# Optimization experiments

Measured on AMD Instinct MI355X. Metric: run time of the kernel, lower is better.

The kernel has to match this reference:

```python
import jax, jax.numpy as jnp
import numpy as np


def setup_inputs() -> dict:
    key = jax.random.key(0)
    k1, k2 = jax.random.split(key)
    B, N, M, C = 4, 8192, 8192, 3
    ref = jax.random.normal(k1, (B, N, C), dtype=jnp.float32)
    query = jax.random.normal(k2, (B, M, C), dtype=jnp.float32)
    return {"ref": ref, "query": query, "k": 16}


def reference(ref, query, k):
    # ref:   [B, N, C] reference points
    # query: [B, M, C] query points
    # Squared Euclidean distances via ||q||^2 + ||r||^2 - 2 q.r  -> [B, M, N]
    q_sq = jnp.sum(query * query, axis=-1, keepdims=True)          # [B, M, 1]
    r_sq = jnp.sum(ref * ref, axis=-1)[:, None, :]                 # [B, 1, N]
    cross = jnp.einsum("bmc,bnc->bmn", query, ref)                 # [B, M, N]
    d2 = jnp.maximum(q_sq + r_sq - 2.0 * cross, 0.0)
    # k smallest distances, sorted ascending (knn_cuda convention)
    neg_topk, idx = jax.lax.top_k(-d2, k)                          # [B, M, k]
    dist = jnp.sqrt(-neg_topk)
    return dist, idx
```

## Files before the change

### kernel.cpp

```cpp
#include <hip/hip_runtime.h>


#define TPB 128
#define QPB 16
#define SPL 8
#define KK 16
#define TILE_PTS 512
#define CAP 16
#define TRIG 8

typedef unsigned long long u64k;
typedef float f32x2 __attribute__((ext_vector_type(2)));

__device__ __forceinline__ f32x2 pk_mul(f32x2 a, f32x2 b) {
  f32x2 d;
  asm("v_pk_mul_f32 %0, %1, %2" : "=v"(d) : "v"(a), "v"(b));
  return d;
}
__device__ __forceinline__ f32x2 pk_fma(f32x2 a, f32x2 b, f32x2 c) {
  f32x2 d;
  asm("v_pk_fma_f32 %0, %1, %2, %3" : "=v"(d) : "v"(a), "v"(b), "v"(c));
  return d;
}
__device__ __forceinline__ f32x2 pk_add(f32x2 a, f32x2 b) {
  f32x2 d;
  asm("v_pk_add_f32 %0, %1, %2" : "=v"(d) : "v"(a), "v"(b));
  return d;
}

#define CE(x, i, j)                                   \
  {                                                   \
    u64k ki_ = x[i], kj_ = x[j];                      \
    bool c_ = kj_ < ki_;                              \
    x[i] = c_ ? kj_ : ki_;                            \
    x[j] = c_ ? ki_ : kj_;                            \
  }

__device__ __forceinline__ void sort16(u64k x[KK]) {
  CE(x,0,1) CE(x,2,3) CE(x,4,5) CE(x,6,7) CE(x,8,9) CE(x,10,11) CE(x,12,13) CE(x,14,15)
  CE(x,0,2) CE(x,1,3) CE(x,4,6) CE(x,5,7) CE(x,8,10) CE(x,9,11) CE(x,12,14) CE(x,13,15)
  CE(x,1,2) CE(x,5,6) CE(x,9,10) CE(x,13,14)
  CE(x,0,4) CE(x,1,5) CE(x,2,6) CE(x,3,7) CE(x,8,12) CE(x,9,13) CE(x,10,14) CE(x,11,15)
  CE(x,2,4) CE(x,3,5) CE(x,10,12) CE(x,11,13)
  CE(x,1,2) CE(x,3,4) CE(x,5,6) CE(x,9,10) CE(x,11,12) CE(x,13,14)
  CE(x,0,8) CE(x,1,9) CE(x,2,10) CE(x,3,11) CE(x,4,12) CE(x,5,13) CE(x,6,14) CE(x,7,15)
  CE(x,4,8) CE(x,5,9) CE(x,6,10) CE(x,7,11)
  CE(x,2,4) CE(x,3,5) CE(x,6,8) CE(x,7,9) CE(x,10,12) CE(x,11,13)
  CE(x,1,2) CE(x,3,4) CE(x,5,6) CE(x,7,8) CE(x,9,10) CE(x,11,12) CE(x,13,14)
}

__device__ __forceinline__ void mergeTop16(u64k a[KK], u64k e[KK]) {
#pragma unroll
  for (int i = 0; i < KK; ++i) {
    u64k bv = e[KK - 1 - i];
    if (bv < a[i]) a[i] = bv;
  }
  CE(a,0,8) CE(a,1,9) CE(a,2,10) CE(a,3,11) CE(a,4,12) CE(a,5,13) CE(a,6,14) CE(a,7,15)
  CE(a,0,4) CE(a,1,5) CE(a,2,6) CE(a,3,7) CE(a,8,12) CE(a,9,13) CE(a,10,14) CE(a,11,15)
  CE(a,0,2) CE(a,1,3) CE(a,4,6) CE(a,5,7) CE(a,8,10) CE(a,9,11) CE(a,12,14) CE(a,13,15)
  CE(a,0,1) CE(a,2,3) CE(a,4,5) CE(a,6,7) CE(a,8,9) CE(a,10,11) CE(a,12,13) CE(a,14,15)
}

__global__ __launch_bounds__(TPB, 4) void knn_topk_kernel(
    const float* __restrict__ ref, const float* __restrict__ query,
    float* __restrict__ dout, float* __restrict__ iout, int N, int M) {
#pragma clang fp contract(off)
  __shared__ float tx[TILE_PTS], ty[TILE_PTS], tz[TILE_PTS], tw[TILE_PTS];
  __shared__ unsigned int sd[CAP * TPB];
  __shared__ unsigned short sg[CAP * TPB];

  float4* tx4 = (float4*)tx;
  float4* ty4 = (float4*)ty;
  float4* tz4 = (float4*)tz;
  float4* tw4 = (float4*)tw;

  const int tid = threadIdx.x;
  const int h = tid & (SPL - 1);
  const int qid = blockIdx.x * QPB + (tid >> 3);
  const int b = qid / M;

  const float* qp = query + (size_t)qid * 3;
  const float qx = qp[0], qy = qp[1], qz = qp[2];
  const float q2 = (qx * qx + qz * qz) + qy * qy;
  const f32x2 qxx = {qx, qx}, qyy = {qy, qy}, qzz = {qz, qz};
  const f32x2 q22 = {q2, q2}, n22 = {-2.0f, -2.0f};

  u64k kl[KK];
  float T;
  int cnt = 0;

  const float* refb = ref + (size_t)b * N * 3;

  auto compact = [&]() {
    u64k e[KK];
#pragma unroll
    for (int s = 0; s < KK; ++s) {
      unsigned int db = sd[s * TPB + tid];
      unsigned int gi = sg[s * TPB + tid];
      u64k key = ((u64k)db << 32) | gi;
      e[s] = (s < cnt) ? key : ~0ull;
    }
    sort16(e);
    mergeTop16(kl, e);
    cnt = 0;
    float a15 = __uint_as_float((unsigned)(kl[KK - 1] >> 32));
    float m = fminf(a15, __shfl_xor(a15, 1));
    m = fminf(m, __shfl_xor(m, 2));
    T = fminf(m, __shfl_xor(m, 4));
  };

  auto evalg = [&](int j, f32x2& d01, f32x2& d23) {
    int ridx = (h << 4) + (j ^ h);
    float4 xs = tx4[ridx];
    float4 ys = ty4[ridx];
    float4 zs = tz4[ridx];
    float4 ws = tw4[ridx];
    f32x2 x01 = {xs.x, xs.y}, x23 = {xs.z, xs.w};
    f32x2 y01 = {ys.x, ys.y}, y23 = {ys.z, ys.w};
    f32x2 z01 = {zs.x, zs.y}, z23 = {zs.z, zs.w};
    f32x2 w01 = {ws.x, ws.y}, w23 = {ws.z, ws.w};
    f32x2 cr01 = pk_mul(qxx, x01);
    cr01 = pk_fma(qyy, y01, cr01);
    cr01 = pk_fma(qzz, z01, cr01);
    f32x2 s01 = pk_add(q22, w01);
    d01 = pk_fma(n22, cr01, s01);
    f32x2 cr23 = pk_mul(qxx, x23);
    cr23 = pk_fma(qyy, y23, cr23);
    cr23 = pk_fma(qzz, z23, cr23);
    f32x2 s23 = pk_add(q22, w23);
    d23 = pk_fma(n22, cr23, s23);
  };

  auto app = [&](float d2, int gi) {
    if (d2 <= T) {
      float d2c = d2 < 0.f ? 0.f : d2;
      sd[cnt * TPB + tid] = __float_as_uint(d2c);
      sg[cnt * TPB + tid] = (unsigned short)gi;
      cnt++;
    }
  };

  const int ntiles = N / TILE_PTS;
  for (int t = 0; t < ntiles; ++t) {
    __syncthreads();
    {
      int pl = tid * 4;
      const float4* rp =
          (const float4*)(refb + (size_t)(t * TILE_PTS + pl) * 3);
      float4 f0 = rp[0], f1 = rp[1], f2 = rp[2];
      float x0 = f0.x, y0 = f0.y, z0 = f0.z;
      float x1 = f0.w, y1 = f1.x, z1 = f1.y;
      float x2 = f1.z, y2 = f1.w, z2 = f2.x;
      float x3 = f2.y, y3 = f2.z, z3 = f2.w;
      int widx = ((tid >> 4) << 4) + ((tid & 15) ^ (tid >> 4));
      tx4[widx] = make_float4(x0, x1, x2, x3);
      ty4[widx] = make_float4(y0, y1, y2, y3);
      tz4[widx] = make_float4(z0, z1, z2, z3);
      tw4[widx] = make_float4((x0 * x0 + z0 * z0) + y0 * y0,
                              (x1 * x1 + z1 * z1) + y1 * y1,
                              (x2 * x2 + z2 * z2) + y2 * y2,
                              (x3 * x3 + z3 * z3) + y3 * y3);
    }
    __syncthreads();
    const int tbase = t * TILE_PTS;
    int j0 = 0;
    if (t == 0) {
#pragma unroll
      for (int j = 0; j < 4; ++j) {
        f32x2 d01, d23;
        evalg(j, d01, d23);
        int gb = (h << 6) + (j << 2);
        float v0 = d01.x < 0.f ? 0.f : d01.x;
        float v1 = d01.y < 0.f ? 0.f : d01.y;
        float v2 = d23.x < 0.f ? 0.f : d23.x;
        float v3 = d23.y < 0.f ? 0.f : d23.y;
        kl[j * 4 + 0] = ((u64k)__float_as_uint(v0) << 32) | (unsigned)(gb + 0);
        kl[j * 4 + 1] = ((u64k)__float_as_uint(v1) << 32) | (unsigned)(gb + 1);
        kl[j * 4 + 2] = ((u64k)__float_as_uint(v2) << 32) | (unsigned)(gb + 2);
        kl[j * 4 + 3] = ((u64k)__float_as_uint(v3) << 32) | (unsigned)(gb + 3);
      }
      sort16(kl);
      float a15 = __uint_as_float((unsigned)(kl[KK - 1] >> 32));
      float m = fminf(a15, __shfl_xor(a15, 1));
      m = fminf(m, __shfl_xor(m, 2));
      T = fminf(m, __shfl_xor(m, 4));
      j0 = 4;
    }
    for (int j = j0; j < TILE_PTS / SPL / 4; j += 2) {
      {
        f32x2 d01, d23;
        evalg(j, d01, d23);
        int gb = tbase + (h << 6) + (j << 2);
        app(d01.x, gb + 0);
        app(d01.y, gb + 1);
        app(d23.x, gb + 2);
        app(d23.y, gb + 3);
      }
      {
        f32x2 d01, d23;
        evalg(j + 1, d01, d23);
        int gb = tbase + (h << 6) + ((j + 1) << 2);
        app(d01.x, gb + 0);
        app(d01.y, gb + 1);
        app(d23.x, gb + 2);
        app(d23.y, gb + 3);
      }
      if (__any(cnt >= TRIG)) compact();
    }
  }
  if (__any(cnt > 0)) compact();

#pragma unroll
  for (int d = 1; d < SPL; d <<= 1) {
    u64k r[KK];
#pragma unroll
    for (int s = 0; s < KK; ++s) r[s] = __shfl_xor(kl[s], d);
    mergeTop16(kl, r);
  }

  if (h == 0) {
    float* dq = dout + (size_t)qid * KK;
    float* iq = iout + (size_t)qid * KK;
    float dv[KK], iv[KK];
#pragma unroll
    for (int o = 0; o < KK; ++o) {
      dv[o] = sqrtf(__uint_as_float((unsigned)(kl[o] >> 32)));
      iv[o] = (float)(unsigned)(kl[o] & 0xffffffffu);
    }
    ((float4*)dq)[0] = make_float4(dv[0], dv[1], dv[2], dv[3]);
    ((float4*)dq)[1] = make_float4(dv[4], dv[5], dv[6], dv[7]);
    ((float4*)dq)[2] = make_float4(dv[8], dv[9], dv[10], dv[11]);
    ((float4*)dq)[3] = make_float4(dv[12], dv[13], dv[14], dv[15]);
    ((float4*)iq)[0] = make_float4(iv[0], iv[1], iv[2], iv[3]);
    ((float4*)iq)[1] = make_float4(iv[4], iv[5], iv[6], iv[7]);
    ((float4*)iq)[2] = make_float4(iv[8], iv[9], iv[10], iv[11]);
    ((float4*)iq)[3] = make_float4(iv[12], iv[13], iv[14], iv[15]);
  }
}

extern "C" void kernel_launch(void* const* d_in, const int* in_sizes, int n_in,
                              void* d_out, int out_size, void* d_ws, size_t ws_size,
                              hipStream_t stream) {
  const float* ref = (const float*)d_in[0];
  const float* query = (const float*)d_in[1];
  const int B = 4, C = 3;
  int N = in_sizes[0] / (B * C);
  int M = in_sizes[1] / (B * C);
  float* dout = (float*)d_out;
  float* iout = dout + (size_t)out_size / 2;
  int totalQ = B * M;
  int blocks = totalQ / QPB;
  knn_topk_kernel<<<blocks, TPB, 0, stream>>>(ref, query, dout, iout, N, M);
}
```

Before: 261.9 us.

## Split each query across 16 lanes with smaller candidate buffers

Doubles the threads per block to 256 and splits each query's reference scan across 16 lanes instead of 8, so each lane covers 32 points per tile. The per-lane candidate buffer shrinks to 8 entries with a trigger of 4, compaction uses an 8-element sort merged into the upper half of the top-16 list, and the threshold reduction gains a fourth shuffle stage. The aim is more parallelism and shorter per-lane serial top-k work. In exchange, compactions happen more often, the final cross-lane merge needs one more round, half the threads sit idle during tile loading, and the larger block raises register and LDS pressure.

```diff
diff --git a/kernel.cpp b/kernel.cpp
--- a/kernel.cpp
+++ b/kernel.cpp
@@ -1,13 +1,13 @@
 #include <hip/hip_runtime.h>
 
 
-#define TPB 128
+#define TPB 256
 #define QPB 16
-#define SPL 8
+#define SPL 16
 #define KK 16
 #define TILE_PTS 512
-#define CAP 16
-#define TRIG 8
+#define CAP 8
+#define TRIG 4
 
 typedef unsigned long long u64k;
 typedef float f32x2 __attribute__((ext_vector_type(2)));
@@ -36,29 +36,38 @@
     x[j] = c_ ? ki_ : kj_;                            \
   }
 
-__device__ __forceinline__ void sort16(u64k x[KK]) {
-  CE(x,0,1) CE(x,2,3) CE(x,4,5) CE(x,6,7) CE(x,8,9) CE(x,10,11) CE(x,12,13) CE(x,14,15)
-  CE(x,0,2) CE(x,1,3) CE(x,4,6) CE(x,5,7) CE(x,8,10) CE(x,9,11) CE(x,12,14) CE(x,13,15)
-  CE(x,1,2) CE(x,5,6) CE(x,9,10) CE(x,13,14)
-  CE(x,0,4) CE(x,1,5) CE(x,2,6) CE(x,3,7) CE(x,8,12) CE(x,9,13) CE(x,10,14) CE(x,11,15)
-  CE(x,2,4) CE(x,3,5) CE(x,10,12) CE(x,11,13)
-  CE(x,1,2) CE(x,3,4) CE(x,5,6) CE(x,9,10) CE(x,11,12) CE(x,13,14)
-  CE(x,0,8) CE(x,1,9) CE(x,2,10) CE(x,3,11) CE(x,4,12) CE(x,5,13) CE(x,6,14) CE(x,7,15)
-  CE(x,4,8) CE(x,5,9) CE(x,6,10) CE(x,7,11)
-  CE(x,2,4) CE(x,3,5) CE(x,6,8) CE(x,7,9) CE(x,10,12) CE(x,11,13)
-  CE(x,1,2) CE(x,3,4) CE(x,5,6) CE(x,7,8) CE(x,9,10) CE(x,11,12) CE(x,13,14)
-}
-
-__device__ __forceinline__ void mergeTop16(u64k a[KK], u64k e[KK]) {
-#pragma unroll
-  for (int i = 0; i < KK; ++i) {
-    u64k bv = e[KK - 1 - i];
-    if (bv < a[i]) a[i] = bv;
-  }
+__device__ __forceinline__ void sort8(u64k x[CAP]) {
+  CE(x,0,1) CE(x,2,3) CE(x,4,5) CE(x,6,7)
+  CE(x,0,2) CE(x,1,3) CE(x,4,6) CE(x,5,7)
+  CE(x,1,2) CE(x,5,6)
+  CE(x,0,4) CE(x,1,5) CE(x,2,6) CE(x,3,7)
+  CE(x,2,4) CE(x,3,5)
+  CE(x,1,2) CE(x,3,4) CE(x,5,6)
+}
+
+__device__ __forceinline__ void clean16(u64k a[KK]) {
   CE(a,0,8) CE(a,1,9) CE(a,2,10) CE(a,3,11) CE(a,4,12) CE(a,5,13) CE(a,6,14) CE(a,7,15)
   CE(a,0,4) CE(a,1,5) CE(a,2,6) CE(a,3,7) CE(a,8,12) CE(a,9,13) CE(a,10,14) CE(a,11,15)
   CE(a,0,2) CE(a,1,3) CE(a,4,6) CE(a,5,7) CE(a,8,10) CE(a,9,11) CE(a,12,14) CE(a,13,15)
   CE(a,0,1) CE(a,2,3) CE(a,4,5) CE(a,6,7) CE(a,8,9) CE(a,10,11) CE(a,12,13) CE(a,14,15)
+}
+
+__device__ __forceinline__ void mergeTop16_8(u64k a[KK], u64k e[CAP]) {
+#pragma unroll
+  for (int i = 0; i < CAP; ++i) {
+    u64k bv = e[CAP - 1 - i];
+    if (bv < a[8 + i]) a[8 + i] = bv;
+  }
+  clean16(a);
+}
+
+__device__ __forceinline__ void mergeTop16(u64k a[KK], u64k e[KK]) {
+#pragma unroll
+  for (int i = 0; i < KK; ++i) {
+    u64k bv = e[KK - 1 - i];
+    if (bv < a[i]) a[i] = bv;
+  }
+  clean16(a);
 }
 
 __global__ __launch_bounds__(TPB, 4) void knn_topk_kernel(
@@ -76,7 +85,7 @@
 
   const int tid = threadIdx.x;
   const int h = tid & (SPL - 1);
-  const int qid = blockIdx.x * QPB + (tid >> 3);
+  const int qid = blockIdx.x * QPB + (tid >> 4);
   const int b = qid / M;
 
   const float* qp = query + (size_t)qid * 3;
@@ -91,26 +100,32 @@
 
   const float* refb = ref + (size_t)b * N * 3;
 
+  auto refreshT = [&]() {
+    float a15 = __uint_as_float((unsigned)(kl[KK - 1] >> 32));
+    float m = fminf(a15, __shfl_xor(a15, 1));
+    m = fminf(m, __shfl_xor(m, 2));
+    m = fminf(m, __shfl_xor(m, 4));
+    T = fminf(m, __shfl_xor(m, 8));
+  };
+
   auto compact = [&]() {
-    u64k e[KK];
-#pragma unroll
-    for (int s = 0; s < KK; ++s) {
+    u64k e[CAP];
+#pragma unroll
+    for (int s = 0; s < CAP; ++s) {
       unsigned int db = sd[s * TPB + tid];
       unsigned int gi = sg[s * TPB + tid];
       u64k key = ((u64k)db << 32) | gi;
       e[s] = (s < cnt) ? key : ~0ull;
     }
-    sort16(e);
-    mergeTop16(kl, e);
+    sort8(e);
+    mergeTop16_8(kl, e);
     cnt = 0;
-    float a15 = __uint_as_float((unsigned)(kl[KK - 1] >> 32));
-    float m = fminf(a15, __shfl_xor(a15, 1));
-    m = fminf(m, __shfl_xor(m, 2));
-    T = fminf(m, __shfl_xor(m, 4));
+    refreshT();
   };
 
   auto evalg = [&](int j, f32x2& d01, f32x2& d23) {
-    int ridx = (h << 4) + (j ^ h);
+    int bb = (h << 3) + j;
+    int ridx = (bb & ~15) | ((bb & 15) ^ (bb >> 4));
     float4 xs = tx4[ridx];
     float4 ys = ty4[ridx];
     float4 zs = tz4[ridx];
@@ -143,7 +158,7 @@
   const int ntiles = N / TILE_PTS;
   for (int t = 0; t < ntiles; ++t) {
     __syncthreads();
-    {
+    if (tid < TILE_PTS / 4) {
       int pl = tid * 4;
       const float4* rp =
           (const float4*)(refb + (size_t)(t * TILE_PTS + pl) * 3);
@@ -169,7 +184,7 @@
       for (int j = 0; j < 4; ++j) {
         f32x2 d01, d23;
         evalg(j, d01, d23);
-        int gb = (h << 6) + (j << 2);
+        int gb = (h << 5) + (j << 2);
         float v0 = d01.x < 0.f ? 0.f : d01.x;
         float v1 = d01.y < 0.f ? 0.f : d01.y;
         float v2 = d23.x < 0.f ? 0.f : d23.x;
@@ -179,32 +194,29 @@
         kl[j * 4 + 2] = ((u64k)__float_as_uint(v2) << 32) | (unsigned)(gb + 2);
         kl[j * 4 + 3] = ((u64k)__float_as_uint(v3) << 32) | (unsigned)(gb + 3);
       }
-      sort16(kl);
-      float a15 = __uint_as_float((unsigned)(kl[KK - 1] >> 32));
-      float m = fminf(a15, __shfl_xor(a15, 1));
-      m = fminf(m, __shfl_xor(m, 2));
-      T = fminf(m, __shfl_xor(m, 4));
+      sort8(kl);
+      sort8(kl + 8);
+      {
+        u64k tmp;
+#pragma unroll
+        for (int i = 0; i < 4; ++i) {
+          tmp = kl[8 + i];
+          kl[8 + i] = kl[15 - i];
+          kl[15 - i] = tmp;
+        }
+        clean16(kl);
+      }
+      refreshT();
       j0 = 4;
     }
-    for (int j = j0; j < TILE_PTS / SPL / 4; j += 2) {
-      {
-        f32x2 d01, d23;
-        evalg(j, d01, d23);
-        int gb = tbase + (h << 6) + (j << 2);
-        app(d01.x, gb + 0);
-        app(d01.y, gb + 1);
-        app(d23.x, gb + 2);
-        app(d23.y, gb + 3);
-      }
-      {
-        f32x2 d01, d23;
-        evalg(j + 1, d01, d23);
-        int gb = tbase + (h << 6) + ((j + 1) << 2);
-        app(d01.x, gb + 0);
-        app(d01.y, gb + 1);
-        app(d23.x, gb + 2);
-        app(d23.y, gb + 3);
-      }
+    for (int j = j0; j < TILE_PTS / SPL / 4; ++j) {
+      f32x2 d01, d23;
+      evalg(j, d01, d23);
+      int gb = tbase + (h << 5) + (j << 2);
+      app(d01.x, gb + 0);
+      app(d01.y, gb + 1);
+      app(d23.x, gb + 2);
+      app(d23.y, gb + 3);
       if (__any(cnt >= TRIG)) compact();
     }
   }
```

Measured after the change: 360.2 us. +37.5%, slower.

## Sort points by norm into bands and prune bands via triangle inequality

Applied to the files above, without the earlier changes.

Adds a prep kernel that bitonic-sorts reference points and queries per batch by squared norm, storing reordered points with their original indices. The main kernel groups queries of similar norm into blocks and starts at the band matching the block's norm. It skips whole 512-point bands when the norm gap exceeds the current k-th distance bound, using the reverse triangle inequality. The prep kernel runs on only 8 blocks with a serial bitonic sort, and the pruned loops add branch divergence. The sorted path is taken only when N and M are 8192 and a large enough workspace is supplied; otherwise the old kernel runs.

```diff
diff --git a/kernel.cpp b/kernel.cpp
--- a/kernel.cpp
+++ b/kernel.cpp
@@ -6,8 +6,9 @@
 #define SPL 8
 #define KK 16
 #define TILE_PTS 512
-#define CAP 16
-#define TRIG 8
+#define NBANDS 16
+#define CAP 14
+#define TRIG 7
 
 typedef unsigned long long u64k;
 typedef float f32x2 __attribute__((ext_vector_type(2)));
@@ -61,13 +62,296 @@
   CE(a,0,1) CE(a,2,3) CE(a,4,5) CE(a,6,7) CE(a,8,9) CE(a,10,11) CE(a,12,13) CE(a,14,15)
 }
 
-__global__ __launch_bounds__(TPB, 4) void knn_topk_kernel(
+
+__device__ __forceinline__ void bitonic8192(u64k* sh, int tid) {
+  for (int k = 2; k <= 8192; k <<= 1) {
+    for (int j = k >> 1; j > 0; j >>= 1) {
+      for (int i = tid; i < 8192; i += 512) {
+        int ixj = i ^ j;
+        if (ixj > i) {
+          u64k a = sh[i], c = sh[ixj];
+          if ((a > c) == ((i & k) == 0)) {
+            sh[i] = c;
+            sh[ixj] = a;
+          }
+        }
+      }
+      __syncthreads();
+    }
+  }
+}
+
+__global__ __launch_bounds__(512) void knn_prep(
+    const float* __restrict__ ref, const float* __restrict__ query,
+    float4* __restrict__ srt, unsigned* __restrict__ sidx,
+    unsigned* __restrict__ qperm, int N, int M) {
+#pragma clang fp contract(off)
+  __shared__ u64k sh[8192];
+  const int tid = threadIdx.x;
+  const int g = blockIdx.x;
+  if (g < 4) {
+    const float* rb = ref + (size_t)g * N * 3;
+    for (int i = tid; i < N; i += 512) {
+      float x = rb[3 * i], y = rb[3 * i + 1], z = rb[3 * i + 2];
+      float r2 = (x * x + z * z) + y * y;
+      sh[i] = ((u64k)__float_as_uint(r2) << 32) | (unsigned)i;
+    }
+    __syncthreads();
+    bitonic8192(sh, tid);
+    for (int s = tid; s < N; s += 512) {
+      u64k key = sh[s];
+      unsigned oi = (unsigned)key;
+      srt[(size_t)g * N + s] =
+          make_float4(rb[3 * oi], rb[3 * oi + 1], rb[3 * oi + 2],
+                      __uint_as_float((unsigned)(key >> 32)));
+      sidx[(size_t)g * N + s] = oi;
+    }
+  } else {
+    const int qb = g - 4;
+    const float* qbp = query + (size_t)qb * M * 3;
+    for (int i = tid; i < M; i += 512) {
+      float x = qbp[3 * i], y = qbp[3 * i + 1], z = qbp[3 * i + 2];
+      float q2 = (x * x + z * z) + y * y;
+      sh[i] = ((u64k)__float_as_uint(q2) << 32) | (unsigned)i;
+    }
+    __syncthreads();
+    bitonic8192(sh, tid);
+    for (int s = tid; s < M; s += 512)
+      qperm[(size_t)qb * M + s] = (unsigned)(qb * M) + (unsigned)sh[s];
+  }
+}
+
+
+__global__ __launch_bounds__(TPB, 4) void knn_main(
+    const float4* __restrict__ srt, const unsigned* __restrict__ sidx,
+    const unsigned* __restrict__ qperm, const float* __restrict__ query,
+    float* __restrict__ dout, float* __restrict__ iout, int N, int M) {
+#pragma clang fp contract(off)
+  __shared__ float tx[TILE_PTS], ty[TILE_PTS], tz[TILE_PTS], tw[TILE_PTS];
+  __shared__ unsigned short ti[TILE_PTS];
+  __shared__ unsigned int sd[CAP * TPB];
+  __shared__ unsigned short sg[CAP * TPB];
+
+  float4* tx4 = (float4*)tx;
+  float4* ty4 = (float4*)ty;
+  float4* tz4 = (float4*)tz;
+  float4* tw4 = (float4*)tw;
+
+  const int tid = threadIdx.x;
+  const int h = tid & (SPL - 1);
+  const int slot = blockIdx.x * QPB + (tid >> 3);
+  const int b = (blockIdx.x * QPB) / M;
+
+  const unsigned orig = qperm[slot];
+  const float* qp = query + (size_t)orig * 3;
+  const float qx = qp[0], qy = qp[1], qz = qp[2];
+  const float q2 = (qx * qx + qz * qz) + qy * qy;
+  const float qn = sqrtf(q2);
+  const f32x2 qxx = {qx, qx}, qyy = {qy, qy}, qzz = {qz, qz};
+  const f32x2 q22 = {q2, q2}, n22 = {-2.0f, -2.0f};
+
+  u64k kl[KK];
+  float T = 3.0e38f;
+  float Ts = 1.8e19f;
+  int cnt = 0;
+
+  const float4* sb = srt + (size_t)b * N;
+  const unsigned* sib = sidx + (size_t)b * N;
+
+  auto refreshT = [&]() {
+    float a15 = __uint_as_float((unsigned)(kl[KK - 1] >> 32));
+    float m = fminf(a15, __shfl_xor(a15, 1));
+    m = fminf(m, __shfl_xor(m, 2));
+    T = fminf(m, __shfl_xor(m, 4));
+    Ts = sqrtf(T) * 1.001f + 0.01f;
+  };
+
+  auto compact = [&]() {
+    u64k e[KK];
+#pragma unroll
+    for (int s = 0; s < KK; ++s) {
+      u64k key = ~0ull;
+      if (s < CAP) {
+        unsigned db = sd[s * TPB + tid];
+        unsigned gi = sg[s * TPB + tid];
+        key = ((u64k)db << 32) | gi;
+      }
+      e[s] = (s < cnt) ? key : ~0ull;
+    }
+    sort16(e);
+    mergeTop16(kl, e);
+    cnt = 0;
+    refreshT();
+  };
+
+  auto evalg = [&](int j, f32x2& d01, f32x2& d23, ushort4& tv) {
+    int ridx = (h << 4) + (j ^ h);
+    float4 xs = tx4[ridx];
+    float4 ys = ty4[ridx];
+    float4 zs = tz4[ridx];
+    float4 ws = tw4[ridx];
+    tv = ((const ushort4*)ti)[ridx];
+    f32x2 x01 = {xs.x, xs.y}, x23 = {xs.z, xs.w};
+    f32x2 y01 = {ys.x, ys.y}, y23 = {ys.z, ys.w};
+    f32x2 z01 = {zs.x, zs.y}, z23 = {zs.z, zs.w};
+    f32x2 w01 = {ws.x, ws.y}, w23 = {ws.z, ws.w};
+    f32x2 cr01 = pk_mul(qxx, x01);
+    cr01 = pk_fma(qyy, y01, cr01);
+    cr01 = pk_fma(qzz, z01, cr01);
+    f32x2 s01 = pk_add(q22, w01);
+    d01 = pk_fma(n22, cr01, s01);
+    f32x2 cr23 = pk_mul(qxx, x23);
+    cr23 = pk_fma(qyy, y23, cr23);
+    cr23 = pk_fma(qzz, z23, cr23);
+    f32x2 s23 = pk_add(q22, w23);
+    d23 = pk_fma(n22, cr23, s23);
+  };
+
+  auto app = [&](float d2, unsigned short oi) {
+    if (d2 <= T) {
+      float d2c = d2 < 0.f ? 0.f : d2;
+      sd[cnt * TPB + tid] = __float_as_uint(d2c);
+      sg[cnt * TPB + tid] = oi;
+      cnt++;
+    }
+  };
+
+  float q2f;
+  {
+    unsigned o0 = qperm[blockIdx.x * QPB];
+    const float* q0 = query + (size_t)o0 * 3;
+    float ax = q0[0], ay = q0[1], az = q0[2];
+    q2f = (ax * ax + az * az) + ay * ay;
+  }
+  int cband = 0;
+  for (int k2 = 1; k2 < NBANDS; ++k2)
+    cband += (sb[(size_t)k2 * TILE_PTS].w <= q2f) ? 1 : 0;
+
+  for (int it = 0; it < NBANDS; ++it) {
+    const int band = (cband + it) & (NBANDS - 1);
+    __syncthreads();
+    {
+      int pl = tid * 4;
+      const float4* rp = sb + (size_t)band * TILE_PTS + pl;
+      float4 p0 = rp[0], p1 = rp[1], p2 = rp[2], p3 = rp[3];
+      const unsigned* ip = sib + (size_t)band * TILE_PTS + pl;
+      unsigned i0 = ip[0], i1 = ip[1], i2 = ip[2], i3 = ip[3];
+      int widx = ((tid >> 4) << 4) + ((tid & 15) ^ (tid >> 4));
+      tx4[widx] = make_float4(p0.x, p1.x, p2.x, p3.x);
+      ty4[widx] = make_float4(p0.y, p1.y, p2.y, p3.y);
+      tz4[widx] = make_float4(p0.z, p1.z, p2.z, p3.z);
+      tw4[widx] = make_float4(p0.w, p1.w, p2.w, p3.w);
+      ((ushort4*)ti)[widx] =
+          make_ushort4((unsigned short)i0, (unsigned short)i1,
+                       (unsigned short)i2, (unsigned short)i3);
+    }
+    __syncthreads();
+    if (it == 0) {
+#pragma unroll
+      for (int j = 0; j < 4; ++j) {
+        f32x2 d01, d23;
+        ushort4 tv;
+        evalg(j, d01, d23, tv);
+        float v0 = d01.x < 0.f ? 0.f : d01.x;
+        float v1 = d01.y < 0.f ? 0.f : d01.y;
+        float v2 = d23.x < 0.f ? 0.f : d23.x;
+        float v3 = d23.y < 0.f ? 0.f : d23.y;
+        kl[j * 4 + 0] = ((u64k)__float_as_uint(v0) << 32) | tv.x;
+        kl[j * 4 + 1] = ((u64k)__float_as_uint(v1) << 32) | tv.y;
+        kl[j * 4 + 2] = ((u64k)__float_as_uint(v2) << 32) | tv.z;
+        kl[j * 4 + 3] = ((u64k)__float_as_uint(v3) << 32) | tv.w;
+      }
+      sort16(kl);
+      refreshT();
+      for (int j = 4; j < 16; j += 2) {
+        {
+          f32x2 d01, d23;
+          ushort4 tv;
+          evalg(j, d01, d23, tv);
+          app(d01.x, tv.x);
+          app(d01.y, tv.y);
+          app(d23.x, tv.z);
+          app(d23.y, tv.w);
+        }
+        {
+          f32x2 d01, d23;
+          ushort4 tv;
+          evalg(j + 1, d01, d23, tv);
+          app(d01.x, tv.x);
+          app(d01.y, tv.y);
+          app(d23.x, tv.z);
+          app(d23.y, tv.w);
+        }
+        if (__any(cnt >= TRIG)) compact();
+      }
+    } else {
+      float lo = sb[(size_t)band * TILE_PTS].w;
+      float hi = sb[(size_t)band * TILE_PTS + TILE_PTS - 1].w;
+      bool skip = (q2 < lo) ? ((sqrtf(lo) - qn) > Ts)
+                            : ((q2 > hi) ? ((qn - sqrtf(hi)) > Ts) : false);
+      if (__any(!skip)) {
+        for (int j = 0; j < 16; j += 2) {
+          {
+            f32x2 d01, d23;
+            ushort4 tv;
+            evalg(j, d01, d23, tv);
+            app(d01.x, tv.x);
+            app(d01.y, tv.y);
+            app(d23.x, tv.z);
+            app(d23.y, tv.w);
+          }
+          {
+            f32x2 d01, d23;
+            ushort4 tv;
+            evalg(j + 1, d01, d23, tv);
+            app(d01.x, tv.x);
+            app(d01.y, tv.y);
+            app(d23.x, tv.z);
+            app(d23.y, tv.w);
+          }
+          if (__any(cnt >= TRIG)) compact();
+        }
+      }
+    }
+  }
+  if (__any(cnt > 0)) compact();
+
+#pragma unroll
+  for (int d = 1; d < SPL; d <<= 1) {
+    u64k r[KK];
+#pragma unroll
+    for (int s = 0; s < KK; ++s) r[s] = __shfl_xor(kl[s], d);
+    mergeTop16(kl, r);
+  }
+
+  if (h == 0) {
+    float* dq = dout + (size_t)orig * KK;
+    float* iq = iout + (size_t)orig * KK;
+    float dv[KK], iv[KK];
+#pragma unroll
+    for (int o = 0; o < KK; ++o) {
+      dv[o] = sqrtf(__uint_as_float((unsigned)(kl[o] >> 32)));
+      iv[o] = (float)(unsigned)(kl[o] & 0xffffffffu);
+    }
+    ((float4*)dq)[0] = make_float4(dv[0], dv[1], dv[2], dv[3]);
+    ((float4*)dq)[1] = make_float4(dv[4], dv[5], dv[6], dv[7]);
+    ((float4*)dq)[2] = make_float4(dv[8], dv[9], dv[10], dv[11]);
+    ((float4*)dq)[3] = make_float4(dv[12], dv[13], dv[14], dv[15]);
+    ((float4*)iq)[0] = make_float4(iv[0], iv[1], iv[2], iv[3]);
+    ((float4*)iq)[1] = make_float4(iv[4], iv[5], iv[6], iv[7]);
+    ((float4*)iq)[2] = make_float4(iv[8], iv[9], iv[10], iv[11]);
+    ((float4*)iq)[3] = make_float4(iv[12], iv[13], iv[14], iv[15]);
+  }
+}
+
+
+__global__ __launch_bounds__(TPB, 4) void knn_legacy(
     const float* __restrict__ ref, const float* __restrict__ query,
     float* __restrict__ dout, float* __restrict__ iout, int N, int M) {
 #pragma clang fp contract(off)
   __shared__ float tx[TILE_PTS], ty[TILE_PTS], tz[TILE_PTS], tw[TILE_PTS];
-  __shared__ unsigned int sd[CAP * TPB];
-  __shared__ unsigned short sg[CAP * TPB];
+  __shared__ unsigned int sd[16 * TPB];
+  __shared__ unsigned short sg[16 * TPB];
 
   float4* tx4 = (float4*)tx;
   float4* ty4 = (float4*)ty;
@@ -86,10 +370,17 @@
   const f32x2 q22 = {q2, q2}, n22 = {-2.0f, -2.0f};
 
   u64k kl[KK];
-  float T;
+  float T = 3.0e38f;
   int cnt = 0;
 
   const float* refb = ref + (size_t)b * N * 3;
+
+  auto refreshT = [&]() {
+    float a15 = __uint_as_float((unsigned)(kl[KK - 1] >> 32));
+    float m = fminf(a15, __shfl_xor(a15, 1));
+    m = fminf(m, __shfl_xor(m, 2));
+    T = fminf(m, __shfl_xor(m, 4));
+  };
 
   auto compact = [&]() {
     u64k e[KK];
@@ -103,10 +394,7 @@
     sort16(e);
     mergeTop16(kl, e);
     cnt = 0;
-    float a15 = __uint_as_float((unsigned)(kl[KK - 1] >> 32));
-    float m = fminf(a15, __shfl_xor(a15, 1));
-    m = fminf(m, __shfl_xor(m, 2));
-    T = fminf(m, __shfl_xor(m, 4));
+    refreshT();
   };
 
   auto evalg = [&](int j, f32x2& d01, f32x2& d23) {
@@ -180,13 +468,10 @@
         kl[j * 4 + 3] = ((u64k)__float_as_uint(v3) << 32) | (unsigned)(gb + 3);
       }
       sort16(kl);
-      float a15 = __uint_as_float((unsigned)(kl[KK - 1] >> 32));
-      float m = fminf(a15, __shfl_xor(a15, 1));
-      m = fminf(m, __shfl_xor(m, 2));
-      T = fminf(m, __shfl_xor(m, 4));
+      refreshT();
       j0 = 4;
     }
-    for (int j = j0; j < TILE_PTS / SPL / 4; j += 2) {
+    for (int j = j0; j < 16; j += 2) {
       {
         f32x2 d01, d23;
         evalg(j, d01, d23);
@@ -205,7 +490,7 @@
         app(d23.x, gb + 2);
         app(d23.y, gb + 3);
       }
-      if (__any(cnt >= TRIG)) compact();
+      if (__any(cnt >= 8)) compact();
     }
   }
   if (__any(cnt > 0)) compact();
@@ -250,5 +535,18 @@
   float* iout = dout + (size_t)out_size / 2;
   int totalQ = B * M;
   int blocks = totalQ / QPB;
-  knn_topk_kernel<<<blocks, TPB, 0, stream>>>(ref, query, dout, iout, N, M);
-}
+  size_t srt_bytes = (size_t)B * N * sizeof(float4);
+  size_t sidx_bytes = (size_t)B * N * sizeof(unsigned);
+  size_t qperm_bytes = (size_t)totalQ * sizeof(unsigned);
+  size_t need = srt_bytes + sidx_bytes + qperm_bytes;
+  if (N == 8192 && M == 8192 && d_ws != nullptr && ws_size >= need) {
+    float4* srt = (float4*)d_ws;
+    unsigned* sidxp = (unsigned*)((char*)d_ws + srt_bytes);
+    unsigned* qpermp = (unsigned*)((char*)d_ws + srt_bytes + sidx_bytes);
+    knn_prep<<<8, 512, 0, stream>>>(ref, query, srt, sidxp, qpermp, N, M);
+    knn_main<<<blocks, TPB, 0, stream>>>(srt, sidxp, qpermp, query, dout, iout,
+                                         N, M);
+  } else {
+    knn_legacy<<<blocks, TPB, 0, stream>>>(ref, query, dout, iout, N, M);
+  }
+}
```

Result: slower. 477.0 us (+82.1%).
